# Kernel tuning notes

Hardware: AMD Instinct MI355X
Metric: run time of the kernel (lower is better)

The kernel has to match this reference:

```python
import jax, jax.numpy as jnp
import numpy as np

C = 32          # middle_channels
N_DOWN = 13     # layers 2..14, stride 2
DENSITY = 0.01  # nnz fraction of the 2048x2048 sparse matrix


def _conv(x, w):
    # centered SAME conv; inactive sites hold zeros so they contribute nothing,
    # matching MinkowskiConvolution's sum over existing neighbor coordinates.
    return jax.lax.conv_general_dilated(
        x, w, window_strides=(1, 1), padding='SAME',
        dimension_numbers=('NHWC', 'HWIO', 'NHWC'))


def _downsample_mask(mask):
    # ME stride-2 output coords = stride-quantized input coords -> OR over 2x2 block
    return jax.lax.reduce_window(mask, 0.0, jax.lax.max, (1, 2, 2), (1, 2, 2), 'SAME')


def _layer(x, mask, w, stride):
    y = _conv(x, w)
    if stride > 1:
        y = y[:, ::stride, ::stride, :]   # value at quantized coordinate u
        mask = _downsample_mask(mask)
    y = jax.nn.relu(y) * mask[..., None]  # ReLU on active sites, keep inactive = 0
    return y, mask


def _global_avg_pool(x, mask):
    cnt = jnp.maximum(jnp.sum(mask, axis=(1, 2)), 1.0)  # number of active coords
    return jnp.sum(x, axis=(1, 2)) / cnt[:, None]       # [B, C]


def setup_inputs() -> dict:
    key = jax.random.key(0)
    ks = jax.random.split(key, 8)
    H = W = 2048
    mask = (jax.random.uniform(ks[0], (1, H, W)) < DENSITY).astype(jnp.float32)
    x = jax.random.normal(ks[1], (1, H, W, 1), dtype=jnp.float32) * mask[..., None]
    # kaiming_normal fan_out (nonlinearity='relu') for conv kernels, bias=False in ME
    w1 = jax.random.normal(ks[2], (5, 5, 1, C), dtype=jnp.float32) * np.float32((2.0 / (5 * 5 * C)) ** 0.5)
    ws = jax.random.normal(ks[3], (N_DOWN, 3, 3, C, C), dtype=jnp.float32) * np.float32((2.0 / (3 * 3 * C)) ** 0.5)
    wm1 = jax.random.normal(ks[4], (C * 14, 256), dtype=jnp.float32) * np.float32((1.0 / (C * 14)) ** 0.5)
    bm1 = jnp.zeros((256,), jnp.float32)
    wm2 = jax.random.normal(ks[5], (256, 128), dtype=jnp.float32) * np.float32((1.0 / 256) ** 0.5)
    bm2 = jnp.zeros((128,), jnp.float32)
    return {'x': x, 'mask': mask, 'w1': w1, 'ws': ws,
            'wm1': wm1, 'bm1': bm1, 'wm2': wm2, 'bm2': bm2}


def reference(x, mask, w1, ws, wm1, bm1, wm2, bm2):
    y, m = _layer(x, mask, w1, stride=1)          # layer1: k=5, s=1
    pools = [_global_avg_pool(y, m)]
    for i in range(N_DOWN):                       # layers 2..14: k=3, s=2
        y, m = _layer(y, m, ws[i], stride=2)
        pools.append(_global_avg_pool(y, m))
    feat = jnp.concatenate(pools, axis=-1)        # [B, 32*14]
    h = jax.nn.relu(feat @ wm1 + bm1)
    return h @ wm2 + bm2                          # [B, 128]
```

## Files before the change

kernel.cpp:

```cpp
#include <hip/hip_runtime.h>

#define NLVL 14
#define NSHARD 16

struct ZeroArgs { unsigned long long zoff[13]; };

__device__ __forceinline__ float fma4(float4 v, float4 w, float acc) {
    acc = fmaf(v.x, w.x, acc);
    acc = fmaf(v.y, w.y, acc);
    acc = fmaf(v.z, w.z, acc);
    return fmaf(v.w, w.w, acc);
}

__device__ __forceinline__ int block_scan_base(int mycnt, int* gcnt, int& myoff) {
    __shared__ int wsum[4];
    __shared__ int base;
    int lane = threadIdx.x & 63, wid = threadIdx.x >> 6;
    int scan = mycnt;
    #pragma unroll
    for (int d = 1; d < 64; d <<= 1) {
        int tv = __shfl_up(scan, d, 64);
        if (lane >= d) scan += tv;
    }
    if (lane == 63) wsum[wid] = scan;
    __syncthreads();
    if (threadIdx.x == 0) {
        int tot = 0;
        #pragma unroll
        for (int i = 0; i < 4; i++) { int tv = wsum[i]; wsum[i] = tot; tot += tv; }
        base = tot ? atomicAdd(gcnt, tot) : 0;
    }
    __syncthreads();
    myoff = wsum[wid] + scan - mycnt;
    return base;
}

__device__ void compact0_tile(const float4* __restrict__ mask4, int* __restrict__ idxmap,
                              int* __restrict__ coords, int* __restrict__ cnt, int cap, int tile) {
    int t = threadIdx.x;
    int g0 = tile * 1024 + t;
    float4 m[4];
    #pragma unroll
    for (int j = 0; j < 4; j++) m[j] = mask4[g0 + j * 256];
    int pr[16];
    int mycnt = 0;
    #pragma unroll
    for (int j = 0; j < 4; j++) {
        pr[4 * j + 0] = m[j].x > 0.5f;
        pr[4 * j + 1] = m[j].y > 0.5f;
        pr[4 * j + 2] = m[j].z > 0.5f;
        pr[4 * j + 3] = m[j].w > 0.5f;
        mycnt += pr[4 * j] + pr[4 * j + 1] + pr[4 * j + 2] + pr[4 * j + 3];
    }
    int myoff;
    int base = block_scan_base(mycnt, cnt, myoff);
    int slot = base + myoff;
    #pragma unroll
    for (int j = 0; j < 4; j++) {
        int e0 = (g0 + j * 256) << 2;
        int wv[4];
        #pragma unroll
        for (int k = 0; k < 4; k++) {
            wv[k] = -1;
            if (pr[4 * j + k]) {
                int sl = slot++;
                if (sl < cap) { wv[k] = sl; coords[sl] = e0 + k; }
            }
        }
        *(int4*)(idxmap + e0) = make_int4(wv[0], wv[1], wv[2], wv[3]);
    }
}

__device__ void down_nbr(const int* __restrict__ idx_in, int HinB,
                         int* __restrict__ idx_out, int* __restrict__ nbr_out,
                         int* __restrict__ cnt_out, int HoutB, int cap_out,
                         int zofs, int bb) {
    int Hout = 1 << HoutB, Hin = 1 << HinB;
    int S = Hout * Hout;
    int S4 = (S + 3) >> 2;
    int o4 = bb * 256 + threadIdx.x;
    int e0 = o4 << 2;
    int jv[4][9];
    int pr[4] = {0, 0, 0, 0};
    #pragma unroll
    for (int k = 0; k < 4; k++)
        #pragma unroll
        for (int tap = 0; tap < 9; tap++) jv[k][tap] = -1;
    if (o4 < S4) {
        if (HoutB >= 2) {
            int r = e0 >> HoutB, c0 = e0 & (Hout - 1);
            int w[3][12];
            #pragma unroll
            for (int a = 0; a < 3; a++) {
                int rr = 2 * r + a - 1;
                bool rok = (unsigned)rr < (unsigned)Hin;
                const int* rowp = idx_in + ((size_t)(rok ? rr : 0) << HinB) + 2 * c0;
                int4 L = (rok && c0 > 0) ? *(const int4*)(rowp - 4) : make_int4(-1, -1, -1, -1);
                int4 M = rok ? *(const int4*)rowp : make_int4(-1, -1, -1, -1);
                int4 R = rok ? *(const int4*)(rowp + 4) : make_int4(-1, -1, -1, -1);
                w[a][0] = L.x; w[a][1] = L.y; w[a][2]  = L.z; w[a][3]  = L.w;
                w[a][4] = M.x; w[a][5] = M.y; w[a][6]  = M.z; w[a][7]  = M.w;
                w[a][8] = R.x; w[a][9] = R.y; w[a][10] = R.z; w[a][11] = R.w;
            }
            #pragma unroll
            for (int k = 0; k < 4; k++) {
                #pragma unroll
                for (int a = 0; a < 3; a++)
                    #pragma unroll
                    for (int b = 0; b < 3; b++)
                        jv[k][a * 3 + b] = w[a][2 * k + b + 3];
                pr[k] = ((jv[k][4] & jv[k][5] & jv[k][7] & jv[k][8]) >= 0);
            }
        } else {
            #pragma unroll
            for (int k = 0; k < 4; k++) {
                int p = e0 + k;
                if (p < S) {
                    int r = p >> HoutB, c = p & (Hout - 1);
                    #pragma unroll
                    for (int a = 0; a < 3; a++)
                        #pragma unroll
                        for (int b = 0; b < 3; b++) {
                            int rr = 2 * r + a - 1, cc = 2 * c + b - 1;
                            if ((unsigned)rr < (unsigned)Hin && (unsigned)cc < (unsigned)Hin)
                                jv[k][a * 3 + b] = idx_in[((size_t)rr << HinB) + cc];
                        }
                    pr[k] = ((jv[k][4] & jv[k][5] & jv[k][7] & jv[k][8]) >= 0);
                }
            }
        }
    }
    int mycnt = pr[0] + pr[1] + pr[2] + pr[3];
    int myoff;
    int base = block_scan_base(mycnt, cnt_out, myoff);
    int slot = base + myoff;
    int wv[4] = {-1, -1, -1, -1};
    #pragma unroll
    for (int k = 0; k < 4; k++) {
        if (pr[k]) {
            int sl = slot++;
            if (sl < cap_out) {
                wv[k] = sl;
                #pragma unroll
                for (int tap = 0; tap < 9; tap++) {
                    int j = jv[k][tap];
                    nbr_out[sl * 9 + tap] = (j < 0) ? zofs : (j << 7);
                }
            }
        }
    }
    if (o4 < S4) {
        if (S >= 4) *(int4*)(idx_out + e0) = make_int4(wv[0], wv[1], wv[2], wv[3]);
        else {
            #pragma unroll
            for (int k = 0; k < 4; k++) if (e0 + k < S) idx_out[e0 + k] = wv[k];
        }
    }
}

__device__ void conv_bs(const char* __restrict__ vprevb, const float* __restrict__ wlvl,
                        const int* __restrict__ nbr, int n,
                        float* __restrict__ vals, float* __restrict__ poolp,
                        int b0, int nbk, int shard) {
    __shared__ int s_j[144];
    __shared__ __align__(16) float s_in[144 * 32];
    int t = threadIdx.x;
    int ciq = t & 7, coh = (t >> 3) & 15, sp = t >> 7;
    float4 wreg[9][2];
    #pragma unroll
    for (int tap = 0; tap < 9; tap++) {
        wreg[tap][0] = *(const float4*)(wlvl + ((tap * 32 + coh) << 5) + (ciq << 2));
        wreg[tap][1] = *(const float4*)(wlvl + ((tap * 32 + coh + 16) << 5) + (ciq << 2));
    }
    float ps0 = 0.f, ps1 = 0.f;
    int ngr = (n + 15) >> 4;
    for (int grp = b0; grp < ngr; grp += nbk) {
        __syncthreads();
        if (t < 144) {
            int gi = grp * 144 + t;
            s_j[t] = (gi < n * 9) ? nbr[gi] : 0;
        }
        __syncthreads();
        #pragma unroll
        for (int i = t; i < 1152; i += 256) {
            int row = i >> 3, q = i & 7;
            *(float4*)&s_in[(row << 5) + (q << 2)] =
                *(const float4*)(vprevb + s_j[row] + (q << 4));
        }
        __syncthreads();
        #pragma unroll
        for (int gp = 0; gp < 8; gp++) {
            int g = gp * 2 + sp;
            int s = (grp << 4) + g;
            float4 v[9];
            #pragma unroll
            for (int tap = 0; tap < 9; tap++)
                v[tap] = *(const float4*)&s_in[((g * 9 + tap) << 5) + (ciq << 2)];
            float a0 = 0.f, a1 = 0.f;
            #pragma unroll
            for (int tap = 0; tap < 9; tap++) {
                a0 = fma4(v[tap], wreg[tap][0], a0);
                a1 = fma4(v[tap], wreg[tap][1], a1);
            }
            a0 += __shfl_xor(a0, 1); a0 += __shfl_xor(a0, 2); a0 += __shfl_xor(a0, 4);
            a1 += __shfl_xor(a1, 1); a1 += __shfl_xor(a1, 2); a1 += __shfl_xor(a1, 4);
            if (ciq == 0 && s < n) {
                float r0 = fmaxf(a0, 0.f), r1 = fmaxf(a1, 0.f);
                vals[((size_t)s << 5) + coh] = r0;
                vals[((size_t)s << 5) + coh + 16] = r1;
                ps0 += r0; ps1 += r1;
            }
        }
    }
    if (ciq == 0 && (ps0 != 0.f || ps1 != 0.f)) {
        atomicAdd(&poolp[shard * 448 + coh], ps0);
        atomicAdd(&poolp[shard * 448 + coh + 16], ps1);
    }
}

__device__ void conv0_bs(const float* __restrict__ x, const float* __restrict__ w1,
                         const int* __restrict__ coords0, int n,
                         float* __restrict__ vals0, float* __restrict__ poolp,
                         int b0, int nbk, int shard) {
    __shared__ float lw[800];
    __shared__ float lx[8][28];
    __shared__ float red[256];
    int t = threadIdx.x;
    for (int i = t; i < 800; i += 256) lw[i] = w1[i];
    int sl = t >> 5, ch = t & 31;
    float psum = 0.f;
    int ngr = (n + 7) >> 3;
    for (int grp = b0; grp < ngr; grp += nbk) {
        __syncthreads();
        if (t < 200) {
            int slot = t / 25, tap = t - slot * 25;
            int s = (grp << 3) + slot;
            float v = 0.f;
            if (s < n) {
                int p = coords0[s];
                int r = p >> 11, c = p & 2047;
                int a = tap / 5, b = tap - a * 5;
                int rr = r + a - 2, cc = c + b - 2;
                if ((unsigned)rr < 2048u && (unsigned)cc < 2048u)
                    v = x[(rr << 11) + cc];
            }
            lx[slot][tap] = v;
        }
        __syncthreads();
        int s = (grp << 3) + sl;
        float acc = 0.f;
        #pragma unroll
        for (int tap = 0; tap < 25; tap++)
            acc = fmaf(lx[sl][tap], lw[tap * 32 + ch], acc);
        if (s < n) {
            float r0 = fmaxf(acc, 0.f);
            vals0[((size_t)s << 5) + ch] = r0;
            psum += r0;
        }
    }
    __syncthreads();
    red[t] = psum;
    __syncthreads();
    if (t < 32) {
        float tot = 0.f;
        #pragma unroll
        for (int q = 0; q < 8; q++) tot += red[t + 32 * q];
        if (tot != 0.f) atomicAdd(&poolp[shard * 448 + t], tot);
    }
}

__global__ __launch_bounds__(256) void k_f0(
    const float4* __restrict__ mask4, int* __restrict__ idxmap,
    int* __restrict__ coords, int* __restrict__ cnt, int cap,
    const float* __restrict__ w, float* __restrict__ wt,
    char* __restrict__ wsbase, ZeroArgs za) {
    if (blockIdx.x == 1492) {
        for (int i = threadIdx.x; i < 13 * 32; i += 256)
            *(float*)(wsbase + za.zoff[i >> 5] + ((i & 31) << 2)) = 0.f;
        return;
    }
    if (blockIdx.x >= 1024) {
        int t = (int)(blockIdx.x - 1024) * 256 + threadIdx.x;
        if (t < 13 * 9 * 32 * 32) {
            int ci = t & 31, co = (t >> 5) & 31, tp = t >> 10;
            wt[(tp << 10) + (co << 5) + ci] = w[(tp << 10) + (ci << 5) + co];
        }
        return;
    }
    compact0_tile(mask4, idxmap, coords, cnt, cap, blockIdx.x);
}

__global__ __launch_bounds__(256) void k_f1(
    const int* __restrict__ idx0, int* __restrict__ idx1, int* __restrict__ nbr1,
    int* __restrict__ cnt1, int cap1, int zofs1,
    const float* __restrict__ x, const float* __restrict__ w1,
    const int* __restrict__ coords0, const int* __restrict__ cnt0, int cap0,
    float* __restrict__ vals0, float* __restrict__ poolp,
    const float* __restrict__ wm1, const float* __restrict__ wm2, float* __restrict__ dummy) {
    if (blockIdx.x < 1024) {
        down_nbr(idx0, 11, idx1, nbr1, cnt1, 10, cap1, zofs1, blockIdx.x);
        return;
    }
    if (blockIdx.x >= 5120) {
        int t = (int)(blockIdx.x - 5120) * 256 + threadIdx.x;
        const float4* a = (const float4*)wm1;
        const float4* b = (const float4*)wm2;
        float acc = 0.f;
        for (int i = t; i < 28672; i += 6144) { float4 v = a[i]; acc += v.x + v.y + v.z + v.w; }
        for (int i = t; i < 8192; i += 6144)  { float4 v = b[i]; acc += v.x + v.y + v.z + v.w; }
        if (acc == 1234.56789f) dummy[0] = acc;
        return;
    }
    int n = *cnt0; if (n > cap0) n = cap0;
    conv0_bs(x, w1, coords0, n, vals0, poolp, blockIdx.x - 1024, 4096, blockIdx.x & (NSHARD - 1));
}

__global__ __launch_bounds__(256) void k_flevel(
    int downB,
    const int* __restrict__ idx_in, int HinB,
    int* __restrict__ idx_out, int* __restrict__ nbr_out, int* __restrict__ cnt_out,
    int HoutB, int cap_out, int zofs,
    const char* __restrict__ vprevb, const float* __restrict__ wlvl,
    const int* __restrict__ nbr_c, const int* __restrict__ cnt_c, int cap_c,
    float* __restrict__ vals_c, float* __restrict__ poolp) {
    if ((int)blockIdx.x < downB) {
        down_nbr(idx_in, HinB, idx_out, nbr_out, cnt_out, HoutB, cap_out, zofs, blockIdx.x);
        return;
    }
    int n = *cnt_c; if (n > cap_c) n = cap_c;
    conv_bs(vprevb, wlvl, nbr_c, n, vals_c, poolp,
            blockIdx.x - downB, gridDim.x - downB, blockIdx.x & (NSHARD - 1));
}

__global__ __launch_bounds__(1024) void k_tail(
    const int* __restrict__ cnt, const float* __restrict__ poolsh,
    const char* __restrict__ vals9b, const int* __restrict__ nbr10,
    const int* __restrict__ idx10, const float* __restrict__ wt,
    const float* __restrict__ wm1, const float* __restrict__ bm1,
    const float* __restrict__ wm2, const float* __restrict__ bm2,
    float* __restrict__ out) {
    __shared__ __align__(16) float v10[128];
    __shared__ float v11[32], v12[32], v13[32];
    __shared__ float feat[448], h[256], part[1024];
    __shared__ int s_i10[4], s_n10;
    int t = threadIdx.x;
    int ciq = t & 7, co = (t >> 3) & 31, s = t >> 8;
    int ciq16 = ciq << 4;
    if (t == 0) s_n10 = cnt[10];
    if (t < 4) s_i10[t] = idx10[t];
    __syncthreads();
    int n10 = s_n10; if (n10 > 4) n10 = 4;
    {
        const float* wl = wt + (size_t)9 * 9216;
        float4 wreg[9];
        #pragma unroll
        for (int tap = 0; tap < 9; tap++)
            wreg[tap] = *(const float4*)(wl + ((tap * 32 + co) << 5) + (ciq << 2));
        bool live = s < n10;
        int sb = live ? s : 0;
        float a0 = 0.f;
        #pragma unroll
        for (int tap = 0; tap < 9; tap++)
            a0 = fma4(*(const float4*)(vals9b + nbr10[sb * 9 + tap] + ciq16), wreg[tap], a0);
        a0 += __shfl_xor(a0, 1); a0 += __shfl_xor(a0, 2); a0 += __shfl_xor(a0, 4);
        if (ciq == 0 && live) v10[s * 32 + co] = fmaxf(a0, 0.f);
    }
    __syncthreads();
    int i10[4] = {s_i10[0], s_i10[1], s_i10[2], s_i10[3]};
    int nbr11[9];
    #pragma unroll
    for (int tap = 0; tap < 9; tap++) {
        int a = tap / 3, b = tap - a * 3;
        int rr = a - 1, cc = b - 1;
        nbr11[tap] = ((unsigned)rr < 2u && (unsigned)cc < 2u) ? i10[rr * 2 + cc] : -1;
    }
    int n11 = ((nbr11[4] & nbr11[5] & nbr11[7] & nbr11[8]) >= 0) ? 1 : 0;
    if (s == 0) {
        const float* wl = wt + (size_t)10 * 9216;
        float a0 = 0.f;
        #pragma unroll
        for (int tap = 0; tap < 9; tap++) {
            int j = nbr11[tap];
            if (j >= 0) {
                float4 wv = *(const float4*)(wl + ((tap * 32 + co) << 5) + (ciq << 2));
                a0 = fma4(*(const float4*)(&v10[(j << 5) + (ciq << 2)]), wv, a0);
            }
        }
        a0 += __shfl_xor(a0, 1); a0 += __shfl_xor(a0, 2); a0 += __shfl_xor(a0, 4);
        if (ciq == 0) v11[co] = n11 ? fmaxf(a0, 0.f) : 0.f;
    }
    __syncthreads();
    if (s == 0) {
        const float* wl = wt + (size_t)11 * 9216;
        float4 wv = *(const float4*)(wl + ((4 * 32 + co) << 5) + (ciq << 2));
        float a0 = n11 ? fma4(*(const float4*)(&v11[ciq << 2]), wv, 0.f) : 0.f;
        a0 += __shfl_xor(a0, 1); a0 += __shfl_xor(a0, 2); a0 += __shfl_xor(a0, 4);
        if (ciq == 0) v12[co] = n11 ? fmaxf(a0, 0.f) : 0.f;
    }
    __syncthreads();
    if (s == 0) {
        const float* wl = wt + (size_t)12 * 9216;
        float4 wv = *(const float4*)(wl + ((4 * 32 + co) << 5) + (ciq << 2));
        float a0 = n11 ? fma4(*(const float4*)(&v12[ciq << 2]), wv, 0.f) : 0.f;
        a0 += __shfl_xor(a0, 1); a0 += __shfl_xor(a0, 2); a0 += __shfl_xor(a0, 4);
        if (ciq == 0) v13[co] = n11 ? fmaxf(a0, 0.f) : 0.f;
    }
    __syncthreads();
    if (t < 320) {
        float sum = 0.f;
        #pragma unroll
        for (int sh = 0; sh < NSHARD; sh++) sum += poolsh[sh * 448 + t];
        float c = (float)cnt[t >> 5]; if (c < 1.f) c = 1.f;
        feat[t] = sum / c;
    }
    if (t < 32) {
        float s10 = 0.f;
        for (int q = 0; q < n10; q++) s10 += v10[q * 32 + t];
        float c10 = (float)n10; if (c10 < 1.f) c10 = 1.f;
        feat[320 + t] = s10 / c10;
        feat[352 + t] = n11 ? v11[t] : 0.f;
        feat[384 + t] = n11 ? v12[t] : 0.f;
        feat[416 + t] = n11 ? v13[t] : 0.f;
    }
    __syncthreads();
    {
        int j = t & 255, chunk = t >> 8;
        float acc = (chunk == 0) ? bm1[j] : 0.f;
        int k0 = chunk * 112;
        #pragma unroll 8
        for (int k = k0; k < k0 + 112; k++) acc = fmaf(feat[k], wm1[k * 256 + j], acc);
        part[t] = acc;
    }
    __syncthreads();
    if (t < 256)
        h[t] = fmaxf(part[t] + part[t + 256] + part[t + 512] + part[t + 768], 0.f);
    __syncthreads();
    {
        int j2 = t & 127, c2 = t >> 7;
        float a2 = (c2 == 0) ? bm2[j2] : 0.f;
        int kk0 = c2 * 32;
        #pragma unroll 8
        for (int k = kk0; k < kk0 + 32; k++) a2 = fmaf(h[k], wm2[k * 128 + j2], a2);
        part[t] = a2;
    }
    __syncthreads();
    if (t < 128) {
        float sum = 0.f;
        #pragma unroll
        for (int c = 0; c < 8; c++) sum += part[t + 128 * c];
        out[t] = sum;
    }
}

extern "C" void kernel_launch(void* const* d_in, const int* in_sizes, int n_in,
                              void* d_out, int out_size, void* d_ws, size_t ws_size,
                              hipStream_t stream) {
    const float* x    = (const float*)d_in[0];
    const float* mask = (const float*)d_in[1];
    const float* w1   = (const float*)d_in[2];
    const float* wsrc = (const float*)d_in[3];
    const float* wm1  = (const float*)d_in[4];
    const float* bm1  = (const float*)d_in[5];
    const float* wm2  = (const float*)d_in[6];
    const float* bm2  = (const float*)d_in[7];
    float* out = (float*)d_out;
    char* ws = (char*)d_ws;

    static const int Hb[NLVL]   = {11, 10, 9, 8, 7, 6, 5, 4, 3, 2, 1, 0, 0, 0};
    static const int caps[NLVL] = {45056, 43008, 43008, 34816, 16384, 4096,
                                   1024, 256, 64, 16, 4, 1, 1, 1};

    size_t pool_off = 256;
    size_t wt_off = 32768;
    size_t off = wt_off + (size_t)13 * 9 * 1024 * 4;
    off = (off + 255) & ~(size_t)255;
    size_t coord0_off = off; off += (size_t)caps[0] * 4; off = (off + 255) & ~(size_t)255;
    size_t idx_off[NLVL], nbr_off[NLVL], val_off[NLVL];
    for (int l = 0; l < NLVL; l++) {
        size_t S = (size_t)(1 << Hb[l]) * (1 << Hb[l]);
        size_t sb = S * 4; if (sb < 16) sb = 16;
        idx_off[l] = off; off += sb; off = (off + 255) & ~(size_t)255;
        if (l >= 1) { nbr_off[l] = off; off += (size_t)caps[l] * 36; off = (off + 255) & ~(size_t)255; }
        else nbr_off[l] = 0;
        val_off[l] = off; off += (size_t)(caps[l] + 1) * 128; off = (off + 255) & ~(size_t)255;
    }

    int* cnt = (int*)ws;
    float* poolsh = (float*)(ws + pool_off);
    float* dummy = (float*)(ws + 128);
    float* wt = (float*)(ws + wt_off);

    ZeroArgs za;
    for (int l = 0; l < 13; l++) za.zoff[l] = val_off[l] + (size_t)caps[l] * 128;

    hipMemsetAsync(ws, 0, 32768, stream);

    k_f0<<<1493, 256, 0, stream>>>(
        (const float4*)mask, (int*)(ws + idx_off[0]), (int*)(ws + coord0_off),
        cnt, caps[0], wsrc, wt, ws, za);

    k_f1<<<5144, 256, 0, stream>>>(
        (const int*)(ws + idx_off[0]), (int*)(ws + idx_off[1]), (int*)(ws + nbr_off[1]),
        cnt + 1, caps[1], caps[0] * 128,
        x, w1, (const int*)(ws + coord0_off), cnt, caps[0],
        (float*)(ws + val_off[0]), poolsh, wm1, wm2, dummy);

    for (int i = 2; i <= 10; i++) {
        int lc = i - 1;
        int Hout = 1 << Hb[i];
        int S4 = (Hout * Hout + 3) >> 2;
        int downB = (S4 + 255) >> 8; if (downB < 1) downB = 1;
        int convB = (caps[lc] + 15) >> 4;
        k_flevel<<<downB + convB, 256, 0, stream>>>(
            downB,
            (const int*)(ws + idx_off[i - 1]), Hb[i - 1],
            (int*)(ws + idx_off[i]), (int*)(ws + nbr_off[i]), cnt + i, Hb[i], caps[i],
            caps[i - 1] * 128,
            (const char*)(ws + val_off[lc - 1]), wt + (size_t)(lc - 1) * 9216,
            (const int*)(ws + nbr_off[lc]), cnt + lc, caps[lc],
            (float*)(ws + val_off[lc]), poolsh + lc * 32);
    }

    k_tail<<<1, 1024, 0, stream>>>(
        cnt, poolsh,
        (const char*)(ws + val_off[9]), (const int*)(ws + nbr_off[10]),
        (const int*)(ws + idx_off[10]), wt,
        wm1, bm1, wm2, bm2, out);
}
```

Baseline: 267.4 us.

## Fold last two sparse levels into single-block tail kernel; widen conv output tiling

```diff
diff --git a/kernel.cpp b/kernel.cpp
--- a/kernel.cpp
+++ b/kernel.cpp
@@ -4,6 +4,17 @@
 #define NSHARD 16
 
 struct ZeroArgs { unsigned long long zoff[13]; };
+
+struct TailArgs {
+    char* ws;
+    const float* wm1; const float* bm1;
+    const float* wm2; const float* bm2;
+    float* out;
+    unsigned long long idx8, idx9, idx10;
+    unsigned long long nbr8, nbr9, nbr10;
+    unsigned long long val7, val8, val9;
+    int cap8, cap9, cap10;
+};
 
 __device__ __forceinline__ float fma4(float4 v, float4 w, float acc) {
     acc = fmaf(v.x, w.x, acc);
@@ -12,9 +23,14 @@
     return fmaf(v.w, w.w, acc);
 }
 
+__device__ __forceinline__ int cnt_load(const int* p) {
+    return __hip_atomic_load(p, __ATOMIC_RELAXED, __HIP_MEMORY_SCOPE_AGENT);
+}
+
 __device__ __forceinline__ int block_scan_base(int mycnt, int* gcnt, int& myoff) {
     __shared__ int wsum[4];
     __shared__ int base;
+    __syncthreads();
     int lane = threadIdx.x & 63, wid = threadIdx.x >> 6;
     int scan = mycnt;
     #pragma unroll
@@ -165,14 +181,14 @@
     __shared__ int s_j[144];
     __shared__ __align__(16) float s_in[144 * 32];
     int t = threadIdx.x;
-    int ciq = t & 7, coh = (t >> 3) & 15, sp = t >> 7;
-    float4 wreg[9][2];
-    #pragma unroll
-    for (int tap = 0; tap < 9; tap++) {
-        wreg[tap][0] = *(const float4*)(wlvl + ((tap * 32 + coh) << 5) + (ciq << 2));
-        wreg[tap][1] = *(const float4*)(wlvl + ((tap * 32 + coh + 16) << 5) + (ciq << 2));
-    }
-    float ps0 = 0.f, ps1 = 0.f;
+    int ciq = t & 7, cog = (t >> 3) & 7, sp = t >> 6;
+    float4 wreg[9][4];
+    #pragma unroll
+    for (int tap = 0; tap < 9; tap++)
+        #pragma unroll
+        for (int q = 0; q < 4; q++)
+            wreg[tap][q] = *(const float4*)(wlvl + ((tap * 32 + cog + 8 * q) << 5) + (ciq << 2));
+    float ps[4] = {0.f, 0.f, 0.f, 0.f};
     int ngr = (n + 15) >> 4;
     for (int grp = b0; grp < ngr; grp += nbk) {
         __syncthreads();
@@ -189,32 +205,39 @@
         }
         __syncthreads();
         #pragma unroll
-        for (int gp = 0; gp < 8; gp++) {
-            int g = gp * 2 + sp;
+        for (int gp = 0; gp < 4; gp++) {
+            int g = gp * 4 + sp;
             int s = (grp << 4) + g;
             float4 v[9];
             #pragma unroll
             for (int tap = 0; tap < 9; tap++)
                 v[tap] = *(const float4*)&s_in[((g * 9 + tap) << 5) + (ciq << 2)];
-            float a0 = 0.f, a1 = 0.f;
+            float a0 = 0.f, a1 = 0.f, a2 = 0.f, a3 = 0.f;
             #pragma unroll
             for (int tap = 0; tap < 9; tap++) {
                 a0 = fma4(v[tap], wreg[tap][0], a0);
                 a1 = fma4(v[tap], wreg[tap][1], a1);
+                a2 = fma4(v[tap], wreg[tap][2], a2);
+                a3 = fma4(v[tap], wreg[tap][3], a3);
             }
             a0 += __shfl_xor(a0, 1); a0 += __shfl_xor(a0, 2); a0 += __shfl_xor(a0, 4);
             a1 += __shfl_xor(a1, 1); a1 += __shfl_xor(a1, 2); a1 += __shfl_xor(a1, 4);
+            a2 += __shfl_xor(a2, 1); a2 += __shfl_xor(a2, 2); a2 += __shfl_xor(a2, 4);
+            a3 += __shfl_xor(a3, 1); a3 += __shfl_xor(a3, 2); a3 += __shfl_xor(a3, 4);
             if (ciq == 0 && s < n) {
                 float r0 = fmaxf(a0, 0.f), r1 = fmaxf(a1, 0.f);
-                vals[((size_t)s << 5) + coh] = r0;
-                vals[((size_t)s << 5) + coh + 16] = r1;
-                ps0 += r0; ps1 += r1;
-            }
-        }
-    }
-    if (ciq == 0 && (ps0 != 0.f || ps1 != 0.f)) {
-        atomicAdd(&poolp[shard * 448 + coh], ps0);
-        atomicAdd(&poolp[shard * 448 + coh + 16], ps1);
+                float r2 = fmaxf(a2, 0.f), r3 = fmaxf(a3, 0.f);
+                float* vp = vals + ((size_t)s << 5) + cog;
+                vp[0] = r0; vp[8] = r1; vp[16] = r2; vp[24] = r3;
+                ps[0] += r0; ps[1] += r1; ps[2] += r2; ps[3] += r3;
+            }
+        }
+    }
+    if (ciq == 0 && (ps[0] != 0.f || ps[1] != 0.f || ps[2] != 0.f || ps[3] != 0.f)) {
+        atomicAdd(&poolp[shard * 448 + cog], ps[0]);
+        atomicAdd(&poolp[shard * 448 + cog + 8], ps[1]);
+        atomicAdd(&poolp[shard * 448 + cog + 16], ps[2]);
+        atomicAdd(&poolp[shard * 448 + cog + 24], ps[3]);
     }
 }
 
@@ -332,21 +355,44 @@
             blockIdx.x - downB, gridDim.x - downB, blockIdx.x & (NSHARD - 1));
 }
 
-__global__ __launch_bounds__(1024) void k_tail(
-    const int* __restrict__ cnt, const float* __restrict__ poolsh,
-    const char* __restrict__ vals9b, const int* __restrict__ nbr10,
-    const int* __restrict__ idx10, const float* __restrict__ wt,
-    const float* __restrict__ wm1, const float* __restrict__ bm1,
-    const float* __restrict__ wm2, const float* __restrict__ bm2,
-    float* __restrict__ out) {
+__global__ __launch_bounds__(256) void k_tail2(TailArgs a) {
+    char* ws = a.ws;
+    int* cnt = (int*)ws;
+    float* poolsh = (float*)(ws + 256);
+    float* wt = (float*)(ws + 32768);
+    int t = threadIdx.x;
+
+    down_nbr((const int*)(ws + a.idx8), 3, (int*)(ws + a.idx9), (int*)(ws + a.nbr9),
+             cnt + 9, 2, a.cap9, a.cap8 * 128, 0);
+    __syncthreads();
+    {
+        int n8 = cnt_load(cnt + 8); if (n8 > a.cap8) n8 = a.cap8;
+        conv_bs((const char*)(ws + a.val7), wt + (size_t)7 * 9216,
+                (const int*)(ws + a.nbr8), n8,
+                (float*)(ws + a.val8), poolsh + 8 * 32, 0, 1, 0);
+    }
+    __syncthreads();
+    down_nbr((const int*)(ws + a.idx9), 2, (int*)(ws + a.idx10), (int*)(ws + a.nbr10),
+             cnt + 10, 1, a.cap10, a.cap9 * 128, 0);
+    __syncthreads();
+    {
+        int n9 = cnt_load(cnt + 9); if (n9 > a.cap9) n9 = a.cap9;
+        conv_bs((const char*)(ws + a.val8), wt + (size_t)8 * 9216,
+                (const int*)(ws + a.nbr9), n9,
+                (float*)(ws + a.val9), poolsh + 9 * 32, 0, 1, 0);
+    }
+    __syncthreads();
+
+    const char* vals9b = (const char*)(ws + a.val9);
+    const int* nbr10 = (const int*)(ws + a.nbr10);
+    const int* idx10 = (const int*)(ws + a.idx10);
     __shared__ __align__(16) float v10[128];
     __shared__ float v11[32], v12[32], v13[32];
-    __shared__ float feat[448], h[256], part[1024];
+    __shared__ float feat[448], h[256], part2[256];
     __shared__ int s_i10[4], s_n10;
-    int t = threadIdx.x;
-    int ciq = t & 7, co = (t >> 3) & 31, s = t >> 8;
+    int ciq = t & 7, co = (t >> 3) & 31;
     int ciq16 = ciq << 4;
-    if (t == 0) s_n10 = cnt[10];
+    if (t == 0) s_n10 = cnt_load(cnt + 10);
     if (t < 4) s_i10[t] = idx10[t];
     __syncthreads();
     int n10 = s_n10; if (n10 > 4) n10 = 4;
@@ -356,26 +402,26 @@
         #pragma unroll
         for (int tap = 0; tap < 9; tap++)
             wreg[tap] = *(const float4*)(wl + ((tap * 32 + co) << 5) + (ciq << 2));
-        bool live = s < n10;
-        int sb = live ? s : 0;
-        float a0 = 0.f;
-        #pragma unroll
-        for (int tap = 0; tap < 9; tap++)
-            a0 = fma4(*(const float4*)(vals9b + nbr10[sb * 9 + tap] + ciq16), wreg[tap], a0);
-        a0 += __shfl_xor(a0, 1); a0 += __shfl_xor(a0, 2); a0 += __shfl_xor(a0, 4);
-        if (ciq == 0 && live) v10[s * 32 + co] = fmaxf(a0, 0.f);
+        for (int s = 0; s < n10; s++) {
+            float a0 = 0.f;
+            #pragma unroll
+            for (int tap = 0; tap < 9; tap++)
+                a0 = fma4(*(const float4*)(vals9b + nbr10[s * 9 + tap] + ciq16), wreg[tap], a0);
+            a0 += __shfl_xor(a0, 1); a0 += __shfl_xor(a0, 2); a0 += __shfl_xor(a0, 4);
+            if (ciq == 0) v10[s * 32 + co] = fmaxf(a0, 0.f);
+        }
     }
     __syncthreads();
     int i10[4] = {s_i10[0], s_i10[1], s_i10[2], s_i10[3]};
     int nbr11[9];
     #pragma unroll
     for (int tap = 0; tap < 9; tap++) {
-        int a = tap / 3, b = tap - a * 3;
-        int rr = a - 1, cc = b - 1;
+        int aa = tap / 3, bb = tap - aa * 3;
+        int rr = aa - 1, cc = bb - 1;
         nbr11[tap] = ((unsigned)rr < 2u && (unsigned)cc < 2u) ? i10[rr * 2 + cc] : -1;
     }
     int n11 = ((nbr11[4] & nbr11[5] & nbr11[7] & nbr11[8]) >= 0) ? 1 : 0;
-    if (s == 0) {
+    {
         const float* wl = wt + (size_t)10 * 9216;
         float a0 = 0.f;
         #pragma unroll
@@ -390,7 +436,7 @@
         if (ciq == 0) v11[co] = n11 ? fmaxf(a0, 0.f) : 0.f;
     }
     __syncthreads();
-    if (s == 0) {
+    {
         const float* wl = wt + (size_t)11 * 9216;
         float4 wv = *(const float4*)(wl + ((4 * 32 + co) << 5) + (ciq << 2));
         float a0 = n11 ? fma4(*(const float4*)(&v11[ciq << 2]), wv, 0.f) : 0.f;
@@ -398,7 +444,7 @@
         if (ciq == 0) v12[co] = n11 ? fmaxf(a0, 0.f) : 0.f;
     }
     __syncthreads();
-    if (s == 0) {
+    {
         const float* wl = wt + (size_t)12 * 9216;
         float4 wv = *(const float4*)(wl + ((4 * 32 + co) << 5) + (ciq << 2));
         float a0 = n11 ? fma4(*(const float4*)(&v12[ciq << 2]), wv, 0.f) : 0.f;
@@ -406,12 +452,12 @@
         if (ciq == 0) v13[co] = n11 ? fmaxf(a0, 0.f) : 0.f;
     }
     __syncthreads();
-    if (t < 320) {
+    for (int j = t; j < 320; j += 256) {
         float sum = 0.f;
         #pragma unroll
-        for (int sh = 0; sh < NSHARD; sh++) sum += poolsh[sh * 448 + t];
-        float c = (float)cnt[t >> 5]; if (c < 1.f) c = 1.f;
-        feat[t] = sum / c;
+        for (int sh = 0; sh < NSHARD; sh++) sum += poolsh[sh * 448 + j];
+        float c = (float)cnt_load(cnt + (j >> 5)); if (c < 1.f) c = 1.f;
+        feat[j] = sum / c;
     }
     if (t < 32) {
         float s10 = 0.f;
@@ -424,32 +470,22 @@
     }
     __syncthreads();
     {
-        int j = t & 255, chunk = t >> 8;
-        float acc = (chunk == 0) ? bm1[j] : 0.f;
-        int k0 = chunk * 112;
+        float acc = a.bm1[t];
         #pragma unroll 8
-        for (int k = k0; k < k0 + 112; k++) acc = fmaf(feat[k], wm1[k * 256 + j], acc);
-        part[t] = acc;
-    }
-    __syncthreads();
-    if (t < 256)
-        h[t] = fmaxf(part[t] + part[t + 256] + part[t + 512] + part[t + 768], 0.f);
+        for (int k = 0; k < 448; k++) acc = fmaf(feat[k], a.wm1[k * 256 + t], acc);
+        h[t] = fmaxf(acc, 0.f);
+    }
     __syncthreads();
     {
         int j2 = t & 127, c2 = t >> 7;
-        float a2 = (c2 == 0) ? bm2[j2] : 0.f;
-        int kk0 = c2 * 32;
+        float a2 = (c2 == 0) ? a.bm2[j2] : 0.f;
+        int kk0 = c2 * 128;
         #pragma unroll 8
-        for (int k = kk0; k < kk0 + 32; k++) a2 = fmaf(h[k], wm2[k * 128 + j2], a2);
-        part[t] = a2;
-    }
-    __syncthreads();
-    if (t < 128) {
-        float sum = 0.f;
-        #pragma unroll
-        for (int c = 0; c < 8; c++) sum += part[t + 128 * c];
-        out[t] = sum;
-    }
+        for (int k = kk0; k < kk0 + 128; k++) a2 = fmaf(h[k], a.wm2[k * 128 + j2], a2);
+        part2[t] = a2;
+    }
+    __syncthreads();
+    if (t < 128) a.out[t] = part2[t] + part2[t + 128];
 }
 
 extern "C" void kernel_launch(void* const* d_in, const int* in_sizes, int n_in,
@@ -505,7 +541,7 @@
         x, w1, (const int*)(ws + coord0_off), cnt, caps[0],
         (float*)(ws + val_off[0]), poolsh, wm1, wm2, dummy);
 
-    for (int i = 2; i <= 10; i++) {
+    for (int i = 2; i <= 8; i++) {
         int lc = i - 1;
         int Hout = 1 << Hb[i];
         int S4 = (Hout * Hout + 3) >> 2;
@@ -521,9 +557,13 @@
             (float*)(ws + val_off[lc]), poolsh + lc * 32);
     }
 
-    k_tail<<<1, 1024, 0, stream>>>(
-        cnt, poolsh,
-        (const char*)(ws + val_off[9]), (const int*)(ws + nbr_off[10]),
-        (const int*)(ws + idx_off[10]), wt,
-        wm1, bm1, wm2, bm2, out);
-}
+    TailArgs ta;
+    ta.ws = ws;
+    ta.wm1 = wm1; ta.bm1 = bm1; ta.wm2 = wm2; ta.bm2 = bm2;
+    ta.out = out;
+    ta.idx8 = idx_off[8];  ta.idx9 = idx_off[9];  ta.idx10 = idx_off[10];
+    ta.nbr8 = nbr_off[8];  ta.nbr9 = nbr_off[9];  ta.nbr10 = nbr_off[10];
+    ta.val7 = val_off[7];  ta.val8 = val_off[8];  ta.val9 = val_off[9];
+    ta.cap8 = caps[8]; ta.cap9 = caps[9]; ta.cap10 = caps[10];
+    k_tail2<<<1, 256, 0, stream>>>(ta);
+}
```

Result: slower. 456.3 us (+70.6%).
